# Kernel optimization log

Hardware: AMD Instinct MI355X
Metric: run time of the kernel (lower is better)

The kernel has to match this reference:

```python
import jax, jax.numpy as jnp
import numpy as np

N = 8192      # number of tree nodes
K = 8         # max degree (8-ary tree)
ALPHA = 64    # alphabet size
DH = 256      # hidden dim


def _lin_w(key, din, dout):
    return jax.random.normal(key, (din, dout), jnp.float32) / np.sqrt(din)


def setup_inputs() -> dict:
    keys = jax.random.split(jax.random.key(0), 24)
    node_types = jax.random.randint(keys[0], (N,), 0, ALPHA, dtype=jnp.int32)
    # deterministic K-ary tree: children of node n are n*K+1 .. n*K+K (if < N)
    idx = np.arange(N)[:, None] * K + 1 + np.arange(K)[None, :]
    mask = idx < N
    children_np = np.where(mask, idx, 0).astype(np.int32)
    A_np = np.zeros((N, N), np.float32)
    A_np[np.repeat(np.arange(N), K)[mask.ravel()], idx.ravel()[mask.ravel()]] = 1.0
    return {
        "node_types": node_types,
        "children": jnp.asarray(children_np),
        "child_mask": jnp.asarray(mask),
        "A": jnp.asarray(A_np),
        # GCN layer params (self-transform + neighbor-transform)
        "Ws0": _lin_w(keys[1], ALPHA, DH), "Wn0": _lin_w(keys[2], ALPHA, DH), "b0": jnp.zeros((DH,), jnp.float32),
        "Ws1": _lin_w(keys[3], DH, DH),    "Wn1": _lin_w(keys[4], DH, DH),    "b1": jnp.zeros((DH,), jnp.float32),
        "Ws2": _lin_w(keys[5], DH, DH),    "Wn2": _lin_w(keys[6], DH, DH),    "b2": jnp.zeros((DH,), jnp.float32),
        # heads
        "we": _lin_w(keys[7], DH, 1), "be": jnp.zeros((1,), jnp.float32),
        "Wt": _lin_w(keys[8], DH, ALPHA), "bt": jnp.zeros((ALPHA,), jnp.float32),
        "ciu_w": _lin_w(keys[9], DH, 1)[:, 0], "ciu_b": jnp.zeros((), jnp.float32),
        "civ_w": _lin_w(keys[10], DH, 1)[:, 0], "civ_b": jnp.zeros((), jnp.float32),
        "ciw_w": jax.random.normal(keys[11], (), jnp.float32), "ciw_b": jnp.zeros((), jnp.float32),
        "cnu_w": _lin_w(keys[12], DH, 1)[:, 0], "cnu_b": jnp.zeros((), jnp.float32),
        "cnv_w": _lin_w(keys[13], DH, 1)[:, 0], "cnv_b": jnp.zeros((), jnp.float32),
        "cnw_w": jax.random.normal(keys[14], (), jnp.float32), "cnw_b": jnp.zeros((), jnp.float32),
    }


def reference(node_types, children, child_mask, A,
              Ws0, Wn0, b0, Ws1, Wn1, b1, Ws2, Wn2, b2,
              we, be, Wt, bt,
              ciu_w, ciu_b, civ_w, civ_b, ciw_w, ciw_b,
              cnu_w, cnu_b, cnv_w, cnv_b, cnw_w, cnw_b):
    X = jax.nn.one_hot(node_types, ALPHA, dtype=jnp.float32)  # [N, ALPHA]

    def gcn(Z, Ws, Wn, b):
        # self transform + adjacency-aggregated neighbor transform
        return Z @ Ws + b + A @ (Z @ Wn)

    H = jax.nn.relu(gcn(X, Ws0, Wn0, b0))
    H = jax.nn.relu(gcn(H, Ws1, Wn1, b1))
    H = jax.nn.relu(gcn(H, Ws2, Wn2, b2))  # [N, DH]

    delta = H @ we + be   # [N, 1] edit scores
    types = H @ Wt + bt   # [N, ALPHA]

    # child index / child num heads only for nodes with delta >= 0.5 and >0 children
    active = (delta[:, 0] >= 0.5) & child_mask.any(-1)
    valid = child_mask & active[:, None]          # [N, K]
    Hc = H[children]                               # [N, K, DH]
    dots = jnp.einsum('nkd,nd->nk', Hc, H)         # [N, K] child-parent products

    s_idx = (H @ ciu_w + ciu_b)[:, None] + (Hc @ civ_w + civ_b) + (ciw_w * dots + ciw_b)
    s_idx = jnp.where(valid, s_idx, 0.0)
    Cidx = jnp.zeros((N, K + 1), jnp.float32).at[:, 0].set(-1.0)
    # scores[i,1:deg+1] = s; scores[i,:deg] -= s  (s is zero-padded past deg)
    Cidx = Cidx.at[:, 1:].add(s_idx).at[:, :K].add(-s_idx)

    s_num = (H @ cnu_w + cnu_b)[:, None] + (Hc @ cnv_w + cnv_b) + (cnw_w * dots + cnw_b)
    Cnum = jnp.where(valid, s_num, 0.0)

    return delta, types, Cidx, Cnum
```

## Files before the change

### kernel.cpp

```cpp
#include <hip/hip_runtime.h>
#include <hip/hip_bf16.h>

#define N 8192
#define KDEG 8
#define ALPHA 64
#define DH 256

typedef unsigned short u16;
typedef __attribute__((ext_vector_type(8))) short short8;
typedef __attribute__((ext_vector_type(4))) float f32x4;
typedef __attribute__((ext_vector_type(4))) unsigned short ushort4_t;
typedef __attribute__((ext_vector_type(8))) unsigned short ushort8_t;

__device__ __forceinline__ float wave_reduce_sum(float v) {
#pragma unroll
    for (int off = 32; off > 0; off >>= 1) v += __shfl_xor(v, off, 64);
    return v;
}
__device__ __forceinline__ u16 bf16_of(float x) {
    __hip_bfloat16 h = __float2bfloat16(x);
    return *(u16*)&h;
}
__device__ __forceinline__ float f_of_bf16(u16 u) {
    __hip_bfloat16 h = *(__hip_bfloat16*)&u;
    return __bfloat162float(h);
}


__global__ __launch_bounds__(256) void k_embed_pack(const int* __restrict__ nt,
    const float* __restrict__ Ws0, const float* __restrict__ Wn0, const float* __restrict__ b0,
    const float* __restrict__ Ws1, const float* __restrict__ Wn1,
    const float* __restrict__ Ws2, const float* __restrict__ Wn2,
    const float* __restrict__ Wt,
    u16* __restrict__ H0hi, u16* __restrict__ H0lo,
    u16* __restrict__ Phi, u16* __restrict__ Plo) {
    int tid = threadIdx.x;
    if (blockIdx.x < 2048) {
        int g = blockIdx.x * 256 + tid;
        int n = g >> 6, d = (g & 63) * 4;
        int t = nt[n];
        f32x4 a = *(const f32x4*)(b0 + d);
        a += *(const f32x4*)(Ws0 + t * DH + d);
        int cb = n * KDEG + 1;
#pragma unroll
        for (int i = 0; i < KDEG; i++) {
            int c = cb + i;
            if (c < N) a += *(const f32x4*)(Wn0 + nt[c] * DH + d);
        }
        ushort4_t hi, lo;
#pragma unroll
        for (int i = 0; i < 4; i++) {
            float x = fmaxf(a[i], 0.f);
            u16 h = bf16_of(x);
            hi[i] = h;
            lo[i] = bf16_of(x - f_of_bf16(h));
        }
        *(ushort4_t*)(H0hi + (size_t)n * DH + d) = hi;
        *(ushort4_t*)(H0lo + (size_t)n * DH + d) = lo;
    } else {
        int e = (blockIdx.x - 2048) * 256 + tid;
        if (e < 262144) {
            int m = e >> 17, o = e & 131071;
            int j = o & 7, l = (o >> 3) & 63, r = o >> 9;
            int kb = r & 15, tt = r >> 4;
            int k = kb * 32 + (l >> 4) * 8 + j;
            int c = tt * 16 + (l & 15);
            const float* W = (k < 256) ? (m ? Ws2 : Ws1) : (m ? Wn2 : Wn1);
            float v = W[(k & 255) * DH + c];
            u16 h = bf16_of(v);
            Phi[e] = h;
            Plo[e] = bf16_of(v - f_of_bf16(h));
        } else if (e < 278528) {
            int o = e - 262144;
            int j = o & 7, l = (o >> 3) & 63, r = o >> 9;
            int kb = r & 7, tt = r >> 3;
            int k = kb * 32 + (l >> 4) * 8 + j;
            int c = tt * 16 + (l & 15);
            float v = Wt[k * ALPHA + c];
            u16 h = bf16_of(v);
            Phi[e] = h;
            Plo[e] = bf16_of(v - f_of_bf16(h));
        }
    }
}

__global__ __launch_bounds__(512) void k_gemm_agg(
    const u16* __restrict__ Hhi, const u16* __restrict__ Hlo,
    u16* __restrict__ Ahi, u16* __restrict__ Alo,
    const u16* __restrict__ Pmhi, const u16* __restrict__ Pmlo,
    const float* __restrict__ bias,
    u16* __restrict__ Ohi, u16* __restrict__ Olo) {
    int tid = threadIdx.x;
    int rg = blockIdx.x;
    if (rg < 64) {
        int i = tid >> 5;
        int cc = (tid & 31) * 8;
        int node = rg * 16 + i;
        int cb = node * KDEG + 1;
        f32x4 s0 = {}, s1 = {};
#pragma unroll
        for (int k = 0; k < KDEG; k++) {
            int c = cb + k;
            if (c < N) {
                ushort8_t hi = *(const ushort8_t*)(Hhi + (size_t)c * DH + cc);
                ushort8_t lo = *(const ushort8_t*)(Hlo + (size_t)c * DH + cc);
#pragma unroll
                for (int q = 0; q < 4; q++) {
                    s0[q] += f_of_bf16(hi[q]) + f_of_bf16(lo[q]);
                    s1[q] += f_of_bf16(hi[4 + q]) + f_of_bf16(lo[4 + q]);
                }
            }
        }
        ushort8_t hi8, lo8;
#pragma unroll
        for (int q = 0; q < 4; q++) {
            u16 h0 = bf16_of(s0[q]); hi8[q] = h0;     lo8[q] = bf16_of(s0[q] - f_of_bf16(h0));
            u16 h1 = bf16_of(s1[q]); hi8[4 + q] = h1; lo8[4 + q] = bf16_of(s1[q] - f_of_bf16(h1));
        }
        *(ushort8_t*)(Ahi + (size_t)node * DH + cc) = hi8;
        *(ushort8_t*)(Alo + (size_t)node * DH + cc) = lo8;
    }
    __syncthreads();

    int cg = tid >> 6;
    int lane = tid & 63;
    int mrow = lane & 15, quad = lane >> 4;
    int row = rg * 16 + mrow;

    const u16* hh = Hhi + (size_t)row * DH + quad * 8;
    const u16* hl = Hlo + (size_t)row * DH + quad * 8;

    f32x4 acc[2] = {};
#pragma unroll
    for (int kb = 0; kb < 8; kb++) {
        short8 ah = *(const short8*)(hh + kb * 32);
        short8 al = *(const short8*)(hl + kb * 32);
#pragma unroll
        for (int ct = 0; ct < 2; ct++) {
            size_t bo = ((size_t)((cg * 2 + ct) * 16 + kb) * 64 + lane) * 8;
            short8 bh = *(const short8*)(Pmhi + bo);
            short8 bl = *(const short8*)(Pmlo + bo);
            acc[ct] = __builtin_amdgcn_mfma_f32_16x16x32_bf16(ah, bh, acc[ct], 0, 0, 0);
            acc[ct] = __builtin_amdgcn_mfma_f32_16x16x32_bf16(ah, bl, acc[ct], 0, 0, 0);
            acc[ct] = __builtin_amdgcn_mfma_f32_16x16x32_bf16(al, bh, acc[ct], 0, 0, 0);
        }
    }
    if (rg < 64) {
        const u16* gh = Ahi + (size_t)row * DH + quad * 8;
        const u16* gl = Alo + (size_t)row * DH + quad * 8;
#pragma unroll
        for (int kb = 0; kb < 8; kb++) {
            short8 ah = *(const short8*)(gh + kb * 32);
            short8 al = *(const short8*)(gl + kb * 32);
#pragma unroll
            for (int ct = 0; ct < 2; ct++) {
                size_t bo = ((size_t)((cg * 2 + ct) * 16 + kb + 8) * 64 + lane) * 8;
                short8 bh = *(const short8*)(Pmhi + bo);
                short8 bl = *(const short8*)(Pmlo + bo);
                acc[ct] = __builtin_amdgcn_mfma_f32_16x16x32_bf16(ah, bh, acc[ct], 0, 0, 0);
                acc[ct] = __builtin_amdgcn_mfma_f32_16x16x32_bf16(ah, bl, acc[ct], 0, 0, 0);
                acc[ct] = __builtin_amdgcn_mfma_f32_16x16x32_bf16(al, bh, acc[ct], 0, 0, 0);
            }
        }
    }
#pragma unroll
    for (int ct = 0; ct < 2; ct++) {
        int col = cg * 32 + ct * 16 + mrow;
        float bb = bias[col];
        int rowb = rg * 16 + quad * 4;
#pragma unroll
        for (int r = 0; r < 4; r++) {
            float x = fmaxf(acc[ct][r] + bb, 0.f);
            u16 h = bf16_of(x);
            Ohi[(size_t)(rowb + r) * DH + col] = h;
            Olo[(size_t)(rowb + r) * DH + col] = bf16_of(x - f_of_bf16(h));
        }
    }
}

__global__ __launch_bounds__(256) void k_heads(const u16* __restrict__ Hhi,
                                               const u16* __restrict__ Hlo,
                                               const u16* __restrict__ Bh,
                                               const u16* __restrict__ Bl,
                                               const float* __restrict__ bt,
                                               const float* __restrict__ we,
                                               const float* __restrict__ be,
                                               const float* __restrict__ ciu_w,
                                               const float* __restrict__ ciu_b,
                                               const float* __restrict__ civ_w,
                                               const float* __restrict__ civ_b,
                                               const float* __restrict__ cnu_w,
                                               const float* __restrict__ cnu_b,
                                               const float* __restrict__ cnv_w,
                                               const float* __restrict__ cnv_b,
                                               const float* __restrict__ ciw_w,
                                               const float* __restrict__ ciw_b,
                                               const float* __restrict__ cnw_w,
                                               const float* __restrict__ cnw_b,
                                               float* __restrict__ delta_out,
                                               float* __restrict__ types_out,
                                               float* __restrict__ cidx_out,
                                               float* __restrict__ cnum_out) {
    int lane = threadIdx.x & 63;
    if (blockIdx.x < 128) {
        int w = blockIdx.x * 4 + (threadIdx.x >> 6);
        int mrow = lane & 15, quad = lane >> 4;
        int r0 = w * 16;
        f32x4 acc[4] = {};
        const u16* ap = Hhi + (size_t)(r0 + mrow) * DH + quad * 8;
        const u16* lp = Hlo + (size_t)(r0 + mrow) * DH + quad * 8;
#pragma unroll
        for (int kb = 0; kb < 8; kb++) {
            short8 ah = *(const short8*)(ap + kb * 32);
            short8 al = *(const short8*)(lp + kb * 32);
#pragma unroll
            for (int ct = 0; ct < 4; ct++) {
                short8 bh = *(const short8*)(Bh + (size_t)((ct * 8 + kb) * 64 + lane) * 8);
                short8 bl = *(const short8*)(Bl + (size_t)((ct * 8 + kb) * 64 + lane) * 8);
                acc[ct] = __builtin_amdgcn_mfma_f32_16x16x32_bf16(ah, bh, acc[ct], 0, 0, 0);
                acc[ct] = __builtin_amdgcn_mfma_f32_16x16x32_bf16(ah, bl, acc[ct], 0, 0, 0);
                acc[ct] = __builtin_amdgcn_mfma_f32_16x16x32_bf16(al, bh, acc[ct], 0, 0, 0);
            }
        }
#pragma unroll
        for (int ct = 0; ct < 4; ct++) {
            float bias = bt[ct * 16 + mrow];
            int rowb = r0 + quad * 4;
#pragma unroll
            for (int r = 0; r < 4; r++)
                types_out[(size_t)(rowb + r) * ALPHA + ct * 16 + mrow] = acc[ct][r] + bias;
        }
    } else {
        int n = (blockIdx.x - 128) * 4 + (threadIdx.x >> 6);
        int j = lane, d = j * 4;
        ushort4_t phi = *(const ushort4_t*)(Hhi + (size_t)n * DH + d);
        ushort4_t plo = *(const ushort4_t*)(Hlo + (size_t)n * DH + d);
        f32x4 hp;
#pragma unroll
        for (int i = 0; i < 4; i++) hp[i] = f_of_bf16(phi[i]) + f_of_bf16(plo[i]);

        f32x4 wd = *(const f32x4*)(we + d);
        float pd = hp[0] * wd[0] + hp[1] * wd[1] + hp[2] * wd[2] + hp[3] * wd[3];
        float delta = wave_reduce_sum(pd) + be[0];
        if (j == 0) delta_out[n] = delta;

        bool active = (delta >= 0.5f) && (n < 1024);
        float my_si = 0.f, my_sn = 0.f;
        if (active) {
            f32x4 w1 = *(const f32x4*)(ciu_w + d);
            f32x4 w3 = *(const f32x4*)(cnu_w + d);
            float ciu_n = wave_reduce_sum(hp[0] * w1[0] + hp[1] * w1[1] +
                                          hp[2] * w1[2] + hp[3] * w1[3]) + ciu_b[0];
            float cnu_n = wave_reduce_sum(hp[0] * w3[0] + hp[1] * w3[1] +
                                          hp[2] * w3[2] + hp[3] * w3[3]) + cnu_b[0];
            f32x4 w2 = *(const f32x4*)(civ_w + d);
            f32x4 w4 = *(const f32x4*)(cnv_w + d);
            float cvb = civ_b[0], nvb = cnv_b[0];
            float iw = ciw_w[0], ib = ciw_b[0], nw = cnw_w[0], nb = cnw_b[0];
#pragma unroll
            for (int k = 0; k < KDEG; k++) {
                int c = n * KDEG + 1 + k;
                float si = 0.f, sn = 0.f;
                if (c < N) {
                    ushort4_t chi = *(const ushort4_t*)(Hhi + (size_t)c * DH + d);
                    ushort4_t clo = *(const ushort4_t*)(Hlo + (size_t)c * DH + d);
                    float p = 0.f, q2 = 0.f, q4 = 0.f;
#pragma unroll
                    for (int i = 0; i < 4; i++) {
                        float hc = f_of_bf16(chi[i]) + f_of_bf16(clo[i]);
                        p += hp[i] * hc;
                        q2 += w2[i] * hc;
                        q4 += w4[i] * hc;
                    }
                    p = wave_reduce_sum(p);
                    q2 = wave_reduce_sum(q2);
                    q4 = wave_reduce_sum(q4);
                    si = ciu_n + (q2 + cvb) + iw * p + ib;
                    sn = cnu_n + (q4 + nvb) + nw * p + nb;
                }
                if (j == k) { my_si = si; my_sn = sn; }
            }
        }
        if (j < KDEG) cnum_out[(size_t)n * KDEG + j] = my_sn;
        float prev = __shfl(my_si, (j >= 1) ? (j - 1) : 0, 64);
        float val;
        if (j == 0)        val = -1.f - my_si;
        else if (j < KDEG) val = prev - my_si;
        else               val = prev;
        if (j <= KDEG) cidx_out[(size_t)n * (KDEG + 1) + j] = val;
    }
}

extern "C" void kernel_launch(void* const* d_in, const int* in_sizes, int n_in,
                              void* d_out, int out_size, void* d_ws, size_t ws_size,
                              hipStream_t stream) {
    const int* nt = (const int*)d_in[0];
    const float* Ws0 = (const float*)d_in[4];
    const float* Wn0 = (const float*)d_in[5];
    const float* b0  = (const float*)d_in[6];
    const float* Ws1 = (const float*)d_in[7];
    const float* Wn1 = (const float*)d_in[8];
    const float* b1  = (const float*)d_in[9];
    const float* Ws2 = (const float*)d_in[10];
    const float* Wn2 = (const float*)d_in[11];
    const float* b2  = (const float*)d_in[12];
    const float* we  = (const float*)d_in[13];
    const float* be  = (const float*)d_in[14];
    const float* Wt  = (const float*)d_in[15];
    const float* bt  = (const float*)d_in[16];
    const float* ciu_w = (const float*)d_in[17];
    const float* ciu_b = (const float*)d_in[18];
    const float* civ_w = (const float*)d_in[19];
    const float* civ_b = (const float*)d_in[20];
    const float* ciw_w = (const float*)d_in[21];
    const float* ciw_b = (const float*)d_in[22];
    const float* cnu_w = (const float*)d_in[23];
    const float* cnu_b = (const float*)d_in[24];
    const float* cnv_w = (const float*)d_in[25];
    const float* cnv_b = (const float*)d_in[26];
    const float* cnw_w = (const float*)d_in[27];
    const float* cnw_b = (const float*)d_in[28];

    char* w = (char*)d_ws;
    u16* H0hi = (u16*)(w);
    u16* H0lo = (u16*)(w + ((size_t)4 << 20));
    u16* H1hi = (u16*)(w + ((size_t)8 << 20));
    u16* H1lo = (u16*)(w + ((size_t)12 << 20));
    u16* H2hi = (u16*)(w + ((size_t)16 << 20));
    u16* H2lo = (u16*)(w + ((size_t)20 << 20));
    u16* A0hi = (u16*)(w + ((size_t)24 << 20));
    u16* A0lo = (u16*)(w + ((size_t)25 << 20));
    u16* A1hi = (u16*)(w + ((size_t)26 << 20));
    u16* A1lo = (u16*)(w + ((size_t)27 << 20));
    u16* Phi  = (u16*)(w + ((size_t)28 << 20));
    u16* Plo  = (u16*)(w + ((size_t)29 << 20));

    float* delta_out = (float*)d_out;
    float* types_out = delta_out + N;
    float* cidx_out  = types_out + (size_t)N * ALPHA;
    float* cnum_out  = cidx_out + (size_t)N * (KDEG + 1);

    k_embed_pack<<<3136, 256, 0, stream>>>(nt, Ws0, Wn0, b0, Ws1, Wn1, Ws2, Wn2, Wt,
                                           H0hi, H0lo, Phi, Plo);
    k_gemm_agg<<<512, 512, 0, stream>>>(H0hi, H0lo, A0hi, A0lo, Phi, Plo, b1, H1hi, H1lo);
    k_gemm_agg<<<512, 512, 0, stream>>>(H1hi, H1lo, A1hi, A1lo,
                                        Phi + 131072, Plo + 131072, b2, H2hi, H2lo);
    k_heads<<<128 + 2048, 256, 0, stream>>>(H2hi, H2lo, Phi + 262144, Plo + 262144, bt,
                                            we, be, ciu_w, ciu_b, civ_w, civ_b,
                                            cnu_w, cnu_b, cnv_w, cnv_b,
                                            ciw_w, ciw_b, cnw_w, cnw_b,
                                            delta_out, types_out, cidx_out, cnum_out);
}
```

Measured before the change: 402.3 us.

## Fuse output heads into last GCN layer epilogue and precompute per-node projections

Moves the types GEMM and the per-node linear projections (delta, ciu, civ, cnu, cnv) into the epilogue of the final gemm_agg kernel. The fp32 H tile is staged in shared memory and re-split to bf16 hi/lo for MFMA. The child kernel then reads the precomputed per-node scalars from an aux buffer instead of recomputing reductions per child, and only handles the 1024 nodes that can have children. Nodes without children get constant outputs written by extra blocks. This removes one kernel pass over H2 and redundant reductions, at the cost of extra shared memory and epilogue work in the last GEMM.

```diff
diff --git a/kernel.cpp b/kernel.cpp
--- a/kernel.cpp
+++ b/kernel.cpp
@@ -84,12 +84,22 @@
     }
 }
 
+template <bool HEADS>
 __global__ __launch_bounds__(512) void k_gemm_agg(
     const u16* __restrict__ Hhi, const u16* __restrict__ Hlo,
     u16* __restrict__ Ahi, u16* __restrict__ Alo,
     const u16* __restrict__ Pmhi, const u16* __restrict__ Pmlo,
     const float* __restrict__ bias,
-    u16* __restrict__ Ohi, u16* __restrict__ Olo) {
+    u16* __restrict__ Ohi, u16* __restrict__ Olo,
+    const u16* __restrict__ Th, const u16* __restrict__ Tl,
+    const float* __restrict__ bt, float* __restrict__ types_out,
+    const float* __restrict__ we, const float* __restrict__ be,
+    const float* __restrict__ ciu_w, const float* __restrict__ ciu_b,
+    const float* __restrict__ civ_w, const float* __restrict__ civ_b,
+    const float* __restrict__ cnu_w, const float* __restrict__ cnu_b,
+    const float* __restrict__ cnv_w, const float* __restrict__ cnv_b,
+    float* __restrict__ aux, float* __restrict__ delta_out) {
+    __shared__ float X[16][265];
     int tid = threadIdx.x;
     int rg = blockIdx.x;
     if (rg < 64) {
@@ -174,88 +184,106 @@
             u16 h = bf16_of(x);
             Ohi[(size_t)(rowb + r) * DH + col] = h;
             Olo[(size_t)(rowb + r) * DH + col] = bf16_of(x - f_of_bf16(h));
-        }
-    }
-}
-
-__global__ __launch_bounds__(256) void k_heads(const u16* __restrict__ Hhi,
+            if (HEADS) X[quad * 4 + r][col] = x;
+        }
+    }
+    if (HEADS) {
+        __syncthreads();
+        if (cg < 2) {
+            f32x4 tacc[2] = {};
+#pragma unroll
+            for (int kb = 0; kb < 8; kb++) {
+                short8 ah, al;
+#pragma unroll
+                for (int j = 0; j < 8; j++) {
+                    float v = X[mrow][kb * 32 + quad * 8 + j];
+                    u16 h = bf16_of(v);
+                    ah[j] = (short)h;
+                    al[j] = (short)bf16_of(v - f_of_bf16(h));
+                }
+#pragma unroll
+                for (int ct2 = 0; ct2 < 2; ct2++) {
+                    int t = cg * 2 + ct2;
+                    size_t bo = ((size_t)(t * 8 + kb) * 64 + lane) * 8;
+                    short8 bh = *(const short8*)(Th + bo);
+                    short8 bl = *(const short8*)(Tl + bo);
+                    tacc[ct2] = __builtin_amdgcn_mfma_f32_16x16x32_bf16(ah, bh, tacc[ct2], 0, 0, 0);
+                    tacc[ct2] = __builtin_amdgcn_mfma_f32_16x16x32_bf16(ah, bl, tacc[ct2], 0, 0, 0);
+                    tacc[ct2] = __builtin_amdgcn_mfma_f32_16x16x32_bf16(al, bh, tacc[ct2], 0, 0, 0);
+                }
+            }
+#pragma unroll
+            for (int ct2 = 0; ct2 < 2; ct2++) {
+                int t = cg * 2 + ct2;
+                float bb = bt[t * 16 + mrow];
+#pragma unroll
+                for (int r = 0; r < 4; r++)
+                    types_out[(size_t)(rg * 16 + quad * 4 + r) * ALPHA + t * 16 + mrow] =
+                        tacc[ct2][r] + bb;
+            }
+        } else {
+            int wv = cg - 2;
+            int j = lane, d = j * 4;
+            f32x4 w0 = *(const f32x4*)(we + d);
+            f32x4 w1 = *(const f32x4*)(ciu_w + d);
+            f32x4 w2 = *(const f32x4*)(civ_w + d);
+            f32x4 w3 = *(const f32x4*)(cnu_w + d);
+            f32x4 w4 = *(const f32x4*)(cnv_w + d);
+            for (int rr = wv; rr < 16; rr += 6) {
+                f32x4 xv = *(const f32x4*)&X[rr][d];
+                float pd = 0.f, p1 = 0.f, p2 = 0.f, p3 = 0.f, p4 = 0.f;
+#pragma unroll
+                for (int i = 0; i < 4; i++) {
+                    pd += xv[i] * w0[i];
+                    p1 += xv[i] * w1[i];
+                    p2 += xv[i] * w2[i];
+                    p3 += xv[i] * w3[i];
+                    p4 += xv[i] * w4[i];
+                }
+                pd = wave_reduce_sum(pd);
+                p1 = wave_reduce_sum(p1);
+                p2 = wave_reduce_sum(p2);
+                p3 = wave_reduce_sum(p3);
+                p4 = wave_reduce_sum(p4);
+                if (j == 0) {
+                    int grow = rg * 16 + rr;
+                    float dv = pd + be[0];
+                    aux[grow * 8 + 0] = dv;
+                    aux[grow * 8 + 1] = p1 + ciu_b[0];
+                    aux[grow * 8 + 2] = p2 + civ_b[0];
+                    aux[grow * 8 + 3] = p3 + cnu_b[0];
+                    aux[grow * 8 + 4] = p4 + cnv_b[0];
+                    delta_out[grow] = dv;
+                }
+            }
+        }
+    }
+}
+
+__global__ __launch_bounds__(256) void k_child(const u16* __restrict__ Hhi,
                                                const u16* __restrict__ Hlo,
-                                               const u16* __restrict__ Bh,
-                                               const u16* __restrict__ Bl,
-                                               const float* __restrict__ bt,
-                                               const float* __restrict__ we,
-                                               const float* __restrict__ be,
-                                               const float* __restrict__ ciu_w,
-                                               const float* __restrict__ ciu_b,
-                                               const float* __restrict__ civ_w,
-                                               const float* __restrict__ civ_b,
-                                               const float* __restrict__ cnu_w,
-                                               const float* __restrict__ cnu_b,
-                                               const float* __restrict__ cnv_w,
-                                               const float* __restrict__ cnv_b,
+                                               const float* __restrict__ aux,
                                                const float* __restrict__ ciw_w,
                                                const float* __restrict__ ciw_b,
                                                const float* __restrict__ cnw_w,
                                                const float* __restrict__ cnw_b,
-                                               float* __restrict__ delta_out,
-                                               float* __restrict__ types_out,
                                                float* __restrict__ cidx_out,
                                                float* __restrict__ cnum_out) {
-    int lane = threadIdx.x & 63;
-    if (blockIdx.x < 128) {
-        int w = blockIdx.x * 4 + (threadIdx.x >> 6);
-        int mrow = lane & 15, quad = lane >> 4;
-        int r0 = w * 16;
-        f32x4 acc[4] = {};
-        const u16* ap = Hhi + (size_t)(r0 + mrow) * DH + quad * 8;
-        const u16* lp = Hlo + (size_t)(r0 + mrow) * DH + quad * 8;
-#pragma unroll
-        for (int kb = 0; kb < 8; kb++) {
-            short8 ah = *(const short8*)(ap + kb * 32);
-            short8 al = *(const short8*)(lp + kb * 32);
-#pragma unroll
-            for (int ct = 0; ct < 4; ct++) {
-                short8 bh = *(const short8*)(Bh + (size_t)((ct * 8 + kb) * 64 + lane) * 8);
-                short8 bl = *(const short8*)(Bl + (size_t)((ct * 8 + kb) * 64 + lane) * 8);
-                acc[ct] = __builtin_amdgcn_mfma_f32_16x16x32_bf16(ah, bh, acc[ct], 0, 0, 0);
-                acc[ct] = __builtin_amdgcn_mfma_f32_16x16x32_bf16(ah, bl, acc[ct], 0, 0, 0);
-                acc[ct] = __builtin_amdgcn_mfma_f32_16x16x32_bf16(al, bh, acc[ct], 0, 0, 0);
-            }
-        }
-#pragma unroll
-        for (int ct = 0; ct < 4; ct++) {
-            float bias = bt[ct * 16 + mrow];
-            int rowb = r0 + quad * 4;
-#pragma unroll
-            for (int r = 0; r < 4; r++)
-                types_out[(size_t)(rowb + r) * ALPHA + ct * 16 + mrow] = acc[ct][r] + bias;
-        }
-    } else {
-        int n = (blockIdx.x - 128) * 4 + (threadIdx.x >> 6);
-        int j = lane, d = j * 4;
-        ushort4_t phi = *(const ushort4_t*)(Hhi + (size_t)n * DH + d);
-        ushort4_t plo = *(const ushort4_t*)(Hlo + (size_t)n * DH + d);
-        f32x4 hp;
-#pragma unroll
-        for (int i = 0; i < 4; i++) hp[i] = f_of_bf16(phi[i]) + f_of_bf16(plo[i]);
-
-        f32x4 wd = *(const f32x4*)(we + d);
-        float pd = hp[0] * wd[0] + hp[1] * wd[1] + hp[2] * wd[2] + hp[3] * wd[3];
-        float delta = wave_reduce_sum(pd) + be[0];
-        if (j == 0) delta_out[n] = delta;
-
-        bool active = (delta >= 0.5f) && (n < 1024);
+    int tid = threadIdx.x;
+    if (blockIdx.x < 256) {
+        int n = blockIdx.x * 4 + (tid >> 6);
+        int j = tid & 63, d = j * 4;
+        float delta = aux[n * 8 + 0];
+        bool active = (delta >= 0.5f);
         float my_si = 0.f, my_sn = 0.f;
         if (active) {
-            f32x4 w1 = *(const f32x4*)(ciu_w + d);
-            f32x4 w3 = *(const f32x4*)(cnu_w + d);
-            float ciu_n = wave_reduce_sum(hp[0] * w1[0] + hp[1] * w1[1] +
-                                          hp[2] * w1[2] + hp[3] * w1[3]) + ciu_b[0];
-            float cnu_n = wave_reduce_sum(hp[0] * w3[0] + hp[1] * w3[1] +
-                                          hp[2] * w3[2] + hp[3] * w3[3]) + cnu_b[0];
-            f32x4 w2 = *(const f32x4*)(civ_w + d);
-            f32x4 w4 = *(const f32x4*)(cnv_w + d);
-            float cvb = civ_b[0], nvb = cnv_b[0];
+            ushort4_t phi = *(const ushort4_t*)(Hhi + (size_t)n * DH + d);
+            ushort4_t plo = *(const ushort4_t*)(Hlo + (size_t)n * DH + d);
+            f32x4 hp;
+#pragma unroll
+            for (int i = 0; i < 4; i++) hp[i] = f_of_bf16(phi[i]) + f_of_bf16(plo[i]);
+            float ciu_n = aux[n * 8 + 1];
+            float cnu_n = aux[n * 8 + 3];
             float iw = ciw_w[0], ib = ciw_b[0], nw = cnw_w[0], nb = cnw_b[0];
 #pragma unroll
             for (int k = 0; k < KDEG; k++) {
@@ -264,19 +292,13 @@
                 if (c < N) {
                     ushort4_t chi = *(const ushort4_t*)(Hhi + (size_t)c * DH + d);
                     ushort4_t clo = *(const ushort4_t*)(Hlo + (size_t)c * DH + d);
-                    float p = 0.f, q2 = 0.f, q4 = 0.f;
-#pragma unroll
-                    for (int i = 0; i < 4; i++) {
-                        float hc = f_of_bf16(chi[i]) + f_of_bf16(clo[i]);
-                        p += hp[i] * hc;
-                        q2 += w2[i] * hc;
-                        q4 += w4[i] * hc;
-                    }
+                    float p = 0.f;
+#pragma unroll
+                    for (int i = 0; i < 4; i++)
+                        p += hp[i] * (f_of_bf16(chi[i]) + f_of_bf16(clo[i]));
                     p = wave_reduce_sum(p);
-                    q2 = wave_reduce_sum(q2);
-                    q4 = wave_reduce_sum(q4);
-                    si = ciu_n + (q2 + cvb) + iw * p + ib;
-                    sn = cnu_n + (q4 + nvb) + nw * p + nb;
+                    si = ciu_n + aux[c * 8 + 2] + iw * p + ib;
+                    sn = cnu_n + aux[c * 8 + 4] + nw * p + nb;
                 }
                 if (j == k) { my_si = si; my_sn = sn; }
             }
@@ -288,6 +310,13 @@
         else if (j < KDEG) val = prev - my_si;
         else               val = prev;
         if (j <= KDEG) cidx_out[(size_t)n * (KDEG + 1) + j] = val;
+    } else {
+        int e = (blockIdx.x - 256) * 256 + tid;
+        if (e < 64512) {
+            cidx_out[9216 + e] = ((e % 9) == 0) ? -1.f : 0.f;
+        } else {
+            cnum_out[8192 + (e - 64512)] = 0.f;
+        }
     }
 }
 
@@ -332,8 +361,9 @@
     u16* A0lo = (u16*)(w + ((size_t)25 << 20));
     u16* A1hi = (u16*)(w + ((size_t)26 << 20));
     u16* A1lo = (u16*)(w + ((size_t)27 << 20));
-    u16* Phi  = (u16*)(w + ((size_t)28 << 20));
-    u16* Plo  = (u16*)(w + ((size_t)29 << 20));
+    float* aux = (float*)(w + ((size_t)28 << 20));
+    u16* Phi  = (u16*)(w + ((size_t)29 << 20));
+    u16* Plo  = (u16*)(w + ((size_t)30 << 20));
 
     float* delta_out = (float*)d_out;
     float* types_out = delta_out + N;
@@ -342,12 +372,19 @@
 
     k_embed_pack<<<3136, 256, 0, stream>>>(nt, Ws0, Wn0, b0, Ws1, Wn1, Ws2, Wn2, Wt,
                                            H0hi, H0lo, Phi, Plo);
-    k_gemm_agg<<<512, 512, 0, stream>>>(H0hi, H0lo, A0hi, A0lo, Phi, Plo, b1, H1hi, H1lo);
-    k_gemm_agg<<<512, 512, 0, stream>>>(H1hi, H1lo, A1hi, A1lo,
-                                        Phi + 131072, Plo + 131072, b2, H2hi, H2lo);
-    k_heads<<<128 + 2048, 256, 0, stream>>>(H2hi, H2lo, Phi + 262144, Plo + 262144, bt,
-                                            we, be, ciu_w, ciu_b, civ_w, civ_b,
-                                            cnu_w, cnu_b, cnv_w, cnv_b,
-                                            ciw_w, ciw_b, cnw_w, cnw_b,
-                                            delta_out, types_out, cidx_out, cnum_out);
-}
+    k_gemm_agg<false><<<512, 512, 0, stream>>>(H0hi, H0lo, A0hi, A0lo, Phi, Plo, b1,
+                                               H1hi, H1lo,
+                                               nullptr, nullptr, nullptr, nullptr,
+                                               nullptr, nullptr, nullptr, nullptr,
+                                               nullptr, nullptr, nullptr, nullptr,
+                                               nullptr, nullptr, nullptr, nullptr);
+    k_gemm_agg<true><<<512, 512, 0, stream>>>(H1hi, H1lo, A1hi, A1lo,
+                                              Phi + 131072, Plo + 131072, b2,
+                                              H2hi, H2lo,
+                                              Phi + 262144, Plo + 262144, bt, types_out,
+                                              we, be, ciu_w, ciu_b, civ_w, civ_b,
+                                              cnu_w, cnu_b, cnv_w, cnv_b,
+                                              aux, delta_out);
+    k_child<<<732, 256, 0, stream>>>(H2hi, H2lo, aux, ciw_w, ciw_b, cnw_w, cnw_b,
+                                     cidx_out, cnum_out);
+}
```

New measurement: 401.5 us. Within noise of the previous version (-0.2%).
